# Optimization experiments

Hardware: AMD Instinct MI355X
Metric: run time of the kernel (lower is better)

## Reference

```python
import jax, jax.numpy as jnp
import numpy as np

EMBED = 1024
HEADS = 16
HEAD_SIZE = EMBED // HEADS


def setup_inputs() -> dict:
    key = jax.random.key(0)
    ks = jax.random.split(key, 11)
    B, S, E = 2, 2048, EMBED
    scale = 1.0 / np.sqrt(E)
    return {
        'q': jax.random.normal(ks[0], (B, S, E), jnp.float32),
        'k': jax.random.normal(ks[1], (B, S, E), jnp.float32),
        'v': jax.random.normal(ks[2], (B, S, E), jnp.float32),
        'Wq': jax.random.normal(ks[3], (E, E), jnp.float32) * scale,
        'bq': jnp.zeros((E,), jnp.float32),
        'Wk': jax.random.normal(ks[4], (E, E), jnp.float32) * scale,
        'bk': jnp.zeros((E,), jnp.float32),
        'Wv': jax.random.normal(ks[5], (E, E), jnp.float32) * scale,
        'bv': jnp.zeros((E,), jnp.float32),
        'Wo': jax.random.normal(ks[6], (E, E), jnp.float32) * scale,
        'bo': jnp.zeros((E,), jnp.float32),
    }


def reference(q, k, v, Wq, bq, Wk, bk, Wv, bv, Wo, bo):
    B, Sq, E = q.shape
    Sk = k.shape[1]
    # linear projections (torch Linear: x @ W.T + b), split into heads
    qh = (q @ Wq.T + bq).reshape(B, Sq, HEADS, HEAD_SIZE)
    kh = (k @ Wk.T + bk).reshape(B, Sk, HEADS, HEAD_SIZE)
    vh = (v @ Wv.T + bv).reshape(B, Sk, HEADS, HEAD_SIZE)
    # NOTE: original scales by 1/sqrt(embed_size), not head_size
    scores = jnp.einsum('bqhe,bkhe->bhqk', qh, kh) / jnp.sqrt(jnp.float32(E))
    probs = jax.nn.softmax(scores, axis=-1)  # dropout eval-mode: identity
    attn = jnp.einsum('bhqk,bkhd->bqhd', probs, vh)
    out = attn.reshape(B, Sq, E) @ Wo.T + bo
    return out
```

## Files before the change

### kernel.cpp

```cpp
#include <hip/hip_runtime.h>


typedef unsigned short u16;
typedef __bf16 bf16x8 __attribute__((ext_vector_type(8)));
typedef float f32x4 __attribute__((ext_vector_type(4)));
typedef u16 u16x4 __attribute__((ext_vector_type(4)));
typedef u16 u16x8 __attribute__((ext_vector_type(8)));

typedef __attribute__((address_space(1))) const unsigned int as1_cu32;
typedef __attribute__((address_space(3))) unsigned int as3_u32;

#if __has_builtin(__builtin_amdgcn_exp2f)
#define EXP2(x) __builtin_amdgcn_exp2f(x)
#else
#define EXP2(x) exp2f(x)
#endif

__device__ __forceinline__ u16 f2bf(float f) {
  unsigned u = __builtin_bit_cast(unsigned, f);
  u += 0x7fffu + ((u >> 16) & 1u);
  return (u16)(u >> 16);
}

__device__ __forceinline__ u16 bfc(float f) {
  return __builtin_bit_cast(u16, (__bf16)f);
}

__device__ __forceinline__ void gl_lds16(const u16* g, u16* l) {
  __builtin_amdgcn_global_load_lds((as1_cu32*)g, (as3_u32*)l, 16, 0, 0);
}

__global__ void cast_kernel(const float* __restrict__ wq, const float* __restrict__ wk,
                            const float* __restrict__ wv, const float* __restrict__ wo,
                            u16* __restrict__ wqb, u16* __restrict__ wkb,
                            u16* __restrict__ wvb, u16* __restrict__ wob) {
  unsigned t = blockIdx.x * 256u + threadIdx.x;
  unsigned which = t >> 18, off = t & 262143u;
  const float* src = which == 0 ? wq : (which == 1 ? wk : (which == 2 ? wv : wo));
  u16* dst = which == 0 ? wqb : (which == 1 ? wkb : (which == 2 ? wvb : wob));
  float4 f = ((const float4*)src)[off];
  u16x4 o;
  o[0] = f2bf(f.x); o[1] = f2bf(f.y); o[2] = f2bf(f.z); o[3] = f2bf(f.w);
  ((u16x4*)dst)[off] = o;
}

template <int MODE, int BM, bool AREG>
__device__ __forceinline__ void gemm_body(const void* __restrict__ Av, const u16* __restrict__ B,
                                          const float* __restrict__ bias, void* __restrict__ Cv,
                                          float scale, char* SMraw) {
  constexpr int MI = BM / 32;
  constexpr int ABUF = BM * 64;
  char* ASM = SMraw;
  char* BSM = SMraw + 2 * ABUF;
  constexpr int N = 1024, NK = 32;
  const int m0 = blockIdx.x * BM;
  const int n0 = blockIdx.y * 128;
  const int tid = threadIdx.x;
  const int w = tid >> 6, l = tid & 63;
  const int lr = l & 15, lg = l >> 4;
  const int wm = (w >> 1) * (BM / 2), wn = (w & 1) * 64;

  auto stageB = [&](int buf, int kt) {
#pragma unroll
    for (int i = 0; i < 2; ++i) {
      const int r0 = i * 64 + w * 16;
      gl_lds16(B + (size_t)(n0 + r0 + (l >> 2)) * 1024 + kt * 32 + (l & 3) * 8,
               (u16*)(BSM + buf * 8192 + r0 * 64));
    }
  };
  auto stageA_dma = [&](int buf, int kt) {
    const u16* A = (const u16*)Av;
#pragma unroll
    for (int i = 0; i < BM / 64; ++i) {
      const int r0 = i * 64 + w * 16;
      gl_lds16(A + (size_t)(m0 + r0 + (l >> 2)) * 1024 + kt * 32 + (l & 3) * 8,
               (u16*)(ASM + buf * ABUF + r0 * 64));
    }
  };
  f32x4 ar[BM / 64][2];
  auto stageA_load = [&](int kt) {
    const float* A = (const float*)Av;
#pragma unroll
    for (int i = 0; i < BM / 64; ++i) {
      const float* src = A + (size_t)(m0 + i * 64 + w * 16 + (l >> 2)) * 1024 + kt * 32 + (l & 3) * 8;
      ar[i][0] = *(const f32x4*)src;
      ar[i][1] = *(const f32x4*)(src + 4);
    }
  };
  auto stageA_write = [&](int buf) {
#pragma unroll
    for (int i = 0; i < BM / 64; ++i) {
      u16x8 v;
#pragma unroll
      for (int j = 0; j < 4; ++j) { v[j] = bfc(ar[i][0][j]); v[4 + j] = bfc(ar[i][1][j]); }
      *(u16x8*)(ASM + buf * ABUF + (i * 64 + w * 16 + (l >> 2)) * 64 + (l & 3) * 16) = v;
    }
  };

  f32x4 acc[MI][4];
#pragma unroll
  for (int i = 0; i < MI; ++i)
#pragma unroll
    for (int j = 0; j < 4; ++j) acc[i][j] = f32x4{0.f, 0.f, 0.f, 0.f};

  if constexpr (AREG) { stageA_load(0); stageA_write(0); }
  else                stageA_dma(0, 0);
  stageB(0, 0);

  for (int kt = 0; kt < NK; ++kt) {
    const int buf = kt & 1;
    __syncthreads();
    if (kt + 1 < NK) {
      if constexpr (AREG) stageA_load(kt + 1);
      else                stageA_dma(buf ^ 1, kt + 1);
      stageB(buf ^ 1, kt + 1);
    }
    bf16x8 af[MI], bfr[4];
#pragma unroll
    for (int i = 0; i < MI; ++i)
      af[i] = *(const bf16x8*)(ASM + buf * ABUF + (wm + i * 16 + lr) * 64 + lg * 16);
#pragma unroll
    for (int i = 0; i < 4; ++i)
      bfr[i] = *(const bf16x8*)(BSM + buf * 8192 + (wn + i * 16 + lr) * 64 + lg * 16);
#pragma unroll
    for (int mi = 0; mi < MI; ++mi)
#pragma unroll
      for (int ni = 0; ni < 4; ++ni)
        acc[mi][ni] = __builtin_amdgcn_mfma_f32_16x16x32_bf16(af[mi], bfr[ni], acc[mi][ni], 0, 0, 0);
    if (kt + 1 < NK) {
      if constexpr (AREG) stageA_write(buf ^ 1);
    }
  }

  float bv[4];
#pragma unroll
  for (int ni = 0; ni < 4; ++ni) bv[ni] = bias[n0 + wn + ni * 16 + lr];

  if constexpr (MODE != 2) {
#pragma unroll
    for (int mi = 0; mi < MI; ++mi)
#pragma unroll
      for (int ni = 0; ni < 4; ++ni)
#pragma unroll
        for (int r = 0; r < 4; ++r) {
          const int row = m0 + wm + mi * 16 + lg * 4 + r;
          const int col = n0 + wn + ni * 16 + lr;
          float vv = (acc[mi][ni][r] + bv[ni]) * scale;
          if constexpr (MODE == 1) ((float*)Cv)[(size_t)row * N + col] = vv;
          else                     ((u16*)Cv)[(size_t)row * N + col] = f2bf(vv);
        }
  } else {
    __syncthreads();
    char* wb = SMraw + w * 8192;
#pragma unroll
    for (int mi = 0; mi < MI; ++mi)
#pragma unroll
      for (int ni = 0; ni < 4; ++ni)
#pragma unroll
        for (int r = 0; r < 4; ++r) {
          const int dl = ni * 16 + lr;
          const int sl = mi * 16 + lg * 4 + r;
          const int phys = (sl >> 3) ^ (lr & 7);
          *(u16*)(wb + dl * 128 + (phys << 4) + (sl & 7) * 2) =
              f2bf(acc[mi][ni][r] + bv[ni]);
        }
    const int sc2 = l & 7, srl2 = l >> 3;
    const int rowg = m0 + wm;
#pragma unroll
    for (int i = 0; i < 8; ++i) {
      const int dl = i * 8 + srl2;
      const int phys = sc2 ^ srl2;
      u16x8 vrow = *(u16x8*)(wb + dl * 128 + (phys << 4));
      const int colg = n0 + wn + dl;
      u16* dst = (u16*)Cv + ((size_t)((rowg >> 11) << 10) + colg) * 2048 +
                 (rowg & 2047) + sc2 * 8;
      *(u16x8*)dst = vrow;
    }
  }
}

__global__ __launch_bounds__(256, 2)
void proj_kernel(const float* __restrict__ q, const float* __restrict__ k, const float* __restrict__ v,
                 const u16* __restrict__ wqb, const u16* __restrict__ wkb, const u16* __restrict__ wvb,
                 const float* __restrict__ bq, const float* __restrict__ bk, const float* __restrict__ bvv,
                 u16* __restrict__ qh, u16* __restrict__ kh, u16* __restrict__ vt) {
  __shared__ __align__(16) char SM[32768];
  if (blockIdx.z == 0)      gemm_body<0, 128, true>(q, wqb, bq, qh, 1.44269504089f / 32.f, SM);
  else if (blockIdx.z == 1) gemm_body<0, 128, true>(k, wkb, bk, kh, 1.0f, SM);
  else                      gemm_body<2, 128, true>(v, wvb, bvv, vt, 1.0f, SM);
}

__global__ __launch_bounds__(256, 2)
void outproj_kernel(const u16* __restrict__ attnb, const u16* __restrict__ wob,
                    const float* __restrict__ bo, float* __restrict__ out) {
  __shared__ __align__(16) char SM[24576];
  gemm_body<1, 64, false>(attnb, wob, bo, out, 1.0f, SM);
}

__global__ __launch_bounds__(256, 2)
void attn_kernel(const u16* __restrict__ Q, const u16* __restrict__ Kh,
                 const u16* __restrict__ Vt, u16* __restrict__ Ao) {
  constexpr int E = 1024, S = 2048, NT = S / 64;
  const int bh = blockIdx.x, qt = blockIdx.y;
  const int b = bh >> 4, h = bh & 15;
  const int tid = threadIdx.x, w = tid >> 6, l = tid & 63;
  const int lr = l & 15, lg = l >> 4;

  __shared__ __align__(16) char SM[32768];

  const u16* Qp = Q + (size_t)b * S * E + (size_t)h * 64;
  const u16* Kp = Kh + (size_t)b * S * E + (size_t)h * 64;
  const u16* Vp = Vt + (size_t)bh * 64 * S;

  const int qbase = qt * 128 + w * 32;
  bf16x8 qa[2][2];
#pragma unroll
  for (int qh = 0; qh < 2; ++qh)
#pragma unroll
    for (int hh = 0; hh < 2; ++hh)
      qa[qh][hh] = *(const bf16x8*)(Qp + (size_t)(qbase + qh * 16 + lr) * E + hh * 32 + lg * 8);

  bf16x8 ones;
#pragma unroll
  for (int j = 0; j < 8; ++j) ones[j] = (__bf16)1.0f;

  f32x4 o_acc[2][4];
#pragma unroll
  for (int qh = 0; qh < 2; ++qh)
#pragma unroll
    for (int nf = 0; nf < 4; ++nf) o_acc[qh][nf] = f32x4{0.f, 0.f, 0.f, 0.f};
  f32x4 sum_acc[2] = {f32x4{0.f, 0.f, 0.f, 0.f}, f32x4{0.f, 0.f, 0.f, 0.f}};

  const int swz8 = lr & 7;
  int fofs0[4], fofs1[4];
#pragma unroll
  for (int nf = 0; nf < 4; ++nf) {
    fofs0[nf] = (((nf * 16 + lr) * 64) + (lg ^ swz8) * 8) * 2;
    fofs1[nf] = (((nf * 16 + lr) * 64) + ((4 + lg) ^ swz8) * 8) * 2;
  }

  const int sc = l & 7, srl = l >> 3;
  auto kperm = [](int r) {
    return (r & 35) | ((r & 12) << 1) | ((r & 16) >> 2);
  };
  auto stageK = [&](int buf, int kb) {
#pragma unroll
    for (int i = 0; i < 2; ++i) {
      const int row = i * 32 + w * 8 + srl;
      const int cp = sc ^ (row & 7);
      gl_lds16(Kp + (size_t)(kb + kperm(row)) * E + cp * 8,
               (u16*)(SM + buf * 8192 + (i * 32 + w * 8) * 128));
    }
  };
  auto stageV = [&](int buf, int kb) {
#pragma unroll
    for (int i = 0; i < 2; ++i) {
      const int row = i * 32 + w * 8 + srl;
      const int cp = sc ^ (row & 7);
      gl_lds16(Vp + (size_t)row * S + kb + cp * 8,
               (u16*)(SM + 16384 + buf * 8192 + (i * 32 + w * 8) * 128));
    }
  };

  stageK(0, 0); stageV(0, 0);
  for (int t = 0; t < NT; ++t) {
    const int cur = t & 1;
    __syncthreads();
    if (t + 1 < NT) { stageK(cur ^ 1, (t + 1) * 64); stageV(cur ^ 1, (t + 1) * 64); }
    const char* Kc = SM + cur * 8192;
    const char* Vc = SM + 16384 + cur * 8192;

    f32x4 sfr[2][4];
    __builtin_amdgcn_s_setprio(1);
#pragma unroll
    for (int nf = 0; nf < 4; ++nf) {
      bf16x8 k0 = *(const bf16x8*)(Kc + fofs0[nf]);
      bf16x8 k1 = *(const bf16x8*)(Kc + fofs1[nf]);
#pragma unroll
      for (int qh = 0; qh < 2; ++qh) {
        f32x4 z = f32x4{0.f, 0.f, 0.f, 0.f};
        z = __builtin_amdgcn_mfma_f32_16x16x32_bf16(k0, qa[qh][0], z, 0, 0, 0);
        sfr[qh][nf] = __builtin_amdgcn_mfma_f32_16x16x32_bf16(k1, qa[qh][1], z, 0, 0, 0);
      }
    }
    __builtin_amdgcn_s_setprio(0);

    bf16x8 pa0[2], pa1[2];
#pragma unroll
    for (int qh = 0; qh < 2; ++qh)
#pragma unroll
      for (int r = 0; r < 4; ++r) {
        pa0[qh][r]     = (__bf16)EXP2(sfr[qh][0][r]);
        pa0[qh][4 + r] = (__bf16)EXP2(sfr[qh][1][r]);
        pa1[qh][r]     = (__bf16)EXP2(sfr[qh][2][r]);
        pa1[qh][4 + r] = (__bf16)EXP2(sfr[qh][3][r]);
      }

#pragma unroll
    for (int qh = 0; qh < 2; ++qh) {
      sum_acc[qh] = __builtin_amdgcn_mfma_f32_16x16x32_bf16(pa0[qh], ones, sum_acc[qh], 0, 0, 0);
      sum_acc[qh] = __builtin_amdgcn_mfma_f32_16x16x32_bf16(pa1[qh], ones, sum_acc[qh], 0, 0, 0);
    }

    __builtin_amdgcn_s_setprio(1);
#pragma unroll
    for (int nf = 0; nf < 4; ++nf) {
      bf16x8 vb0 = *(const bf16x8*)(Vc + fofs0[nf]);
      bf16x8 vb1 = *(const bf16x8*)(Vc + fofs1[nf]);
#pragma unroll
      for (int qh = 0; qh < 2; ++qh) {
        o_acc[qh][nf] = __builtin_amdgcn_mfma_f32_16x16x32_bf16(pa0[qh], vb0, o_acc[qh][nf], 0, 0, 0);
        o_acc[qh][nf] = __builtin_amdgcn_mfma_f32_16x16x32_bf16(pa1[qh], vb1, o_acc[qh][nf], 0, 0, 0);
      }
    }
    __builtin_amdgcn_s_setprio(0);
  }

#pragma unroll
  for (int qh = 0; qh < 2; ++qh)
#pragma unroll
    for (int r = 0; r < 4; ++r) {
      const float inv = 1.0f / sum_acc[qh][r];
      const size_t row = (size_t)b * S + qbase + qh * 16 + lg * 4 + r;
#pragma unroll
      for (int nf = 0; nf < 4; ++nf)
        Ao[row * E + h * 64 + nf * 16 + lr] = f2bf(o_acc[qh][nf][r] * inv);
    }
}

extern "C" void kernel_launch(void* const* d_in, const int* in_sizes, int n_in,
                              void* d_out, int out_size, void* d_ws, size_t ws_size,
                              hipStream_t stream) {
  const float* q  = (const float*)d_in[0];
  const float* k  = (const float*)d_in[1];
  const float* v  = (const float*)d_in[2];
  const float* Wq = (const float*)d_in[3];
  const float* bq = (const float*)d_in[4];
  const float* Wk = (const float*)d_in[5];
  const float* bk = (const float*)d_in[6];
  const float* Wv = (const float*)d_in[7];
  const float* bv = (const float*)d_in[8];
  const float* Wo = (const float*)d_in[9];
  const float* bo = (const float*)d_in[10];
  float* out = (float*)d_out;

  char* ws = (char*)d_ws;
  u16* attnb = (u16*)(ws);
  u16* wqb = (u16*)(ws + (24u << 20));
  u16* wkb = (u16*)(ws + (26u << 20));
  u16* wvb = (u16*)(ws + (28u << 20));
  u16* wob = (u16*)(ws + (30u << 20));
  u16* qhp = (u16*)(ws + (32u << 20));
  u16* khp = (u16*)(ws + (40u << 20));
  u16* vtp = (u16*)(ws + (48u << 20));

  cast_kernel<<<dim3(4096), dim3(256), 0, stream>>>(Wq, Wk, Wv, Wo, wqb, wkb, wvb, wob);
  proj_kernel<<<dim3(32, 8, 3), dim3(256), 0, stream>>>(q, k, v, wqb, wkb, wvb,
                                                        bq, bk, bv, qhp, khp, vtp);
  attn_kernel<<<dim3(32, 16), dim3(256), 0, stream>>>(qhp, khp, vtp, attnb);
  outproj_kernel<<<dim3(64, 8), dim3(256), 0, stream>>>(attnb, wob, bo, out);
}
```

Baseline: 105.2 us.

## Double GEMM K-tile to 64 and XOR-swizzle LDS tiles

Raises the K depth of each staged GEMM tile from 32 to 64, which halves the main-loop trip count and the number of barriers per output tile in the projection and output-projection kernels. LDS rows grow to 128 bytes, so global-to-LDS staging and fragment reads now use an XOR swizzle on the 16-byte chunk index to avoid bank conflicts. Fragment offsets are precomputed outside the loop. LDS use per block doubles (64KB for proj, 48KB for outproj), which may limit occupancy and raises register pressure for the register-staged A path.

```diff
diff --git a/kernel.cpp b/kernel.cpp
--- a/kernel.cpp
+++ b/kernel.cpp
@@ -49,10 +49,11 @@
                                           const float* __restrict__ bias, void* __restrict__ Cv,
                                           float scale, char* SMraw) {
   constexpr int MI = BM / 32;
-  constexpr int ABUF = BM * 64;
+  constexpr int ABUF = BM * 128;
+  constexpr int BBUF = 128 * 128;
   char* ASM = SMraw;
   char* BSM = SMraw + 2 * ABUF;
-  constexpr int N = 1024, NK = 32;
+  constexpr int N = 1024, NK = 16;
   const int m0 = blockIdx.x * BM;
   const int n0 = blockIdx.y * 128;
   const int tid = threadIdx.x;
@@ -60,42 +61,60 @@
   const int lr = l & 15, lg = l >> 4;
   const int wm = (w >> 1) * (BM / 2), wn = (w & 1) * 64;
 
+  const int srow = l >> 3, spc = l & 7;
+  auto stage_dma = [&](char* dstbase, const u16* Op, int o0, int r0, int kt) {
+    const int row = r0 + srow;
+    const int lc = spc ^ (row & 7);
+    gl_lds16(Op + (size_t)(o0 + row) * 1024 + kt * 64 + lc * 8,
+             (u16*)(dstbase + r0 * 128));
+  };
   auto stageB = [&](int buf, int kt) {
 #pragma unroll
-    for (int i = 0; i < 2; ++i) {
-      const int r0 = i * 64 + w * 16;
-      gl_lds16(B + (size_t)(n0 + r0 + (l >> 2)) * 1024 + kt * 32 + (l & 3) * 8,
-               (u16*)(BSM + buf * 8192 + r0 * 64));
-    }
+    for (int i = 0; i < 4; ++i)
+      stage_dma(BSM + buf * BBUF, B, n0, i * 32 + w * 8, kt);
   };
   auto stageA_dma = [&](int buf, int kt) {
-    const u16* A = (const u16*)Av;
-#pragma unroll
-    for (int i = 0; i < BM / 64; ++i) {
-      const int r0 = i * 64 + w * 16;
-      gl_lds16(A + (size_t)(m0 + r0 + (l >> 2)) * 1024 + kt * 32 + (l & 3) * 8,
-               (u16*)(ASM + buf * ABUF + r0 * 64));
-    }
-  };
-  f32x4 ar[BM / 64][2];
+#pragma unroll
+    for (int i = 0; i < BM / 32; ++i)
+      stage_dma(ASM + buf * ABUF, (const u16*)Av, m0, i * 32 + w * 8, kt);
+  };
+  f32x4 ar[4][2];
   auto stageA_load = [&](int kt) {
     const float* A = (const float*)Av;
 #pragma unroll
-    for (int i = 0; i < BM / 64; ++i) {
-      const float* src = A + (size_t)(m0 + i * 64 + w * 16 + (l >> 2)) * 1024 + kt * 32 + (l & 3) * 8;
-      ar[i][0] = *(const f32x4*)src;
-      ar[i][1] = *(const f32x4*)(src + 4);
+    for (int p = 0; p < 4; ++p) {
+      const int row = p * 32 + w * 8 + srow;
+      const float* src = A + (size_t)(m0 + row) * 1024 + kt * 64 + spc * 8;
+      ar[p][0] = *(const f32x4*)src;
+      ar[p][1] = *(const f32x4*)(src + 4);
     }
   };
   auto stageA_write = [&](int buf) {
 #pragma unroll
-    for (int i = 0; i < BM / 64; ++i) {
+    for (int p = 0; p < 4; ++p) {
+      const int row = p * 32 + w * 8 + srow;
       u16x8 v;
 #pragma unroll
-      for (int j = 0; j < 4; ++j) { v[j] = bfc(ar[i][0][j]); v[4 + j] = bfc(ar[i][1][j]); }
-      *(u16x8*)(ASM + buf * ABUF + (i * 64 + w * 16 + (l >> 2)) * 64 + (l & 3) * 16) = v;
-    }
-  };
+      for (int j = 0; j < 4; ++j) { v[j] = bfc(ar[p][0][j]); v[4 + j] = bfc(ar[p][1][j]); }
+      *(u16x8*)(ASM + buf * ABUF + row * 128 + ((spc ^ (row & 7)) << 4)) = v;
+    }
+  };
+
+  int afo[MI][2], bfo[4][2];
+#pragma unroll
+  for (int i = 0; i < MI; ++i) {
+    const int arow = wm + i * 16 + lr;
+#pragma unroll
+    for (int ks = 0; ks < 2; ++ks)
+      afo[i][ks] = arow * 128 + (((ks * 4 + lg) ^ (arow & 7)) << 4);
+  }
+#pragma unroll
+  for (int i = 0; i < 4; ++i) {
+    const int brow = wn + i * 16 + lr;
+#pragma unroll
+    for (int ks = 0; ks < 2; ++ks)
+      bfo[i][ks] = brow * 128 + (((ks * 4 + lg) ^ (brow & 7)) << 4);
+  }
 
   f32x4 acc[MI][4];
 #pragma unroll
@@ -115,18 +134,21 @@
       else                stageA_dma(buf ^ 1, kt + 1);
       stageB(buf ^ 1, kt + 1);
     }
-    bf16x8 af[MI], bfr[4];
-#pragma unroll
-    for (int i = 0; i < MI; ++i)
-      af[i] = *(const bf16x8*)(ASM + buf * ABUF + (wm + i * 16 + lr) * 64 + lg * 16);
-#pragma unroll
-    for (int i = 0; i < 4; ++i)
-      bfr[i] = *(const bf16x8*)(BSM + buf * 8192 + (wn + i * 16 + lr) * 64 + lg * 16);
-#pragma unroll
-    for (int mi = 0; mi < MI; ++mi)
-#pragma unroll
-      for (int ni = 0; ni < 4; ++ni)
-        acc[mi][ni] = __builtin_amdgcn_mfma_f32_16x16x32_bf16(af[mi], bfr[ni], acc[mi][ni], 0, 0, 0);
+#pragma unroll
+    for (int ks = 0; ks < 2; ++ks) {
+      bf16x8 af[MI], bfr[4];
+#pragma unroll
+      for (int i = 0; i < MI; ++i)
+        af[i] = *(const bf16x8*)(ASM + buf * ABUF + afo[i][ks]);
+#pragma unroll
+      for (int i = 0; i < 4; ++i)
+        bfr[i] = *(const bf16x8*)(BSM + buf * BBUF + bfo[i][ks]);
+#pragma unroll
+      for (int mi = 0; mi < MI; ++mi)
+#pragma unroll
+        for (int ni = 0; ni < 4; ++ni)
+          acc[mi][ni] = __builtin_amdgcn_mfma_f32_16x16x32_bf16(af[mi], bfr[ni], acc[mi][ni], 0, 0, 0);
+    }
     if (kt + 1 < NK) {
       if constexpr (AREG) stageA_write(buf ^ 1);
     }
@@ -184,7 +206,7 @@
                  const u16* __restrict__ wqb, const u16* __restrict__ wkb, const u16* __restrict__ wvb,
                  const float* __restrict__ bq, const float* __restrict__ bk, const float* __restrict__ bvv,
                  u16* __restrict__ qh, u16* __restrict__ kh, u16* __restrict__ vt) {
-  __shared__ __align__(16) char SM[32768];
+  __shared__ __align__(16) char SM[65536];
   if (blockIdx.z == 0)      gemm_body<0, 128, true>(q, wqb, bq, qh, 1.44269504089f / 32.f, SM);
   else if (blockIdx.z == 1) gemm_body<0, 128, true>(k, wkb, bk, kh, 1.0f, SM);
   else                      gemm_body<2, 128, true>(v, wvb, bvv, vt, 1.0f, SM);
@@ -193,7 +215,7 @@
 __global__ __launch_bounds__(256, 2)
 void outproj_kernel(const u16* __restrict__ attnb, const u16* __restrict__ wob,
                     const float* __restrict__ bo, float* __restrict__ out) {
-  __shared__ __align__(16) char SM[24576];
+  __shared__ __align__(16) char SM[49152];
   gemm_body<1, 64, false>(attnb, wob, bo, out, 1.0f, SM);
 }
 
```

Result: slower. 108.0 us (+2.7%).
